# Kernel optimization log

Hardware: AMD Instinct MI355X
Metric: run time of the kernel (lower is better)

## Reference

```python
import jax, jax.numpy as jnp
import numpy as np
import math

B, S, D, H = 2, 1024, 1024, 16
DH = D // H
BUCKETS, MAXPOS = 256, 512
SPAN = BUCKETS  # pos_ebd_size (att_span)


def make_log_bucket_position(rel, bucket_size, max_position):
    sign = jnp.sign(rel).astype(jnp.float32)
    mid = bucket_size // 2
    abs_pos = jnp.where((rel < mid) & (rel > -mid), mid - 1, jnp.abs(rel)).astype(jnp.float32)
    log_pos = jnp.ceil(jnp.log(abs_pos / mid) / np.log((max_position - 1) / mid) * (mid - 1)) + mid
    return jnp.where(abs_pos <= mid, rel.astype(jnp.float32), log_pos * sign).astype(jnp.int32)


def build_relative_position(q_size, k_size):
    rel = jnp.arange(q_size, dtype=jnp.int32)[:, None] - jnp.arange(k_size, dtype=jnp.int32)[None, :]
    return make_log_bucket_position(rel, BUCKETS, MAXPOS)


def setup_inputs() -> dict:
    key = jax.random.key(0)
    ks = jax.random.split(key, 8)
    w = lambda k: jax.random.normal(k, (D, D), dtype=jnp.float32) * 0.02
    return {
        "hidden_states": jax.random.normal(ks[0], (B, S, D), dtype=jnp.float32),
        "attention_mask": jnp.ones((B, 1, S, S), dtype=jnp.int32),
        "rel_embeddings": jax.random.normal(ks[1], (2 * SPAN, D), dtype=jnp.float32),
        "Wq": w(ks[2]), "bq": jnp.zeros((D,), jnp.float32),
        "Wk": w(ks[3]), "bk": jnp.zeros((D,), jnp.float32),
        "Wv": w(ks[4]), "bv": jnp.zeros((D,), jnp.float32),
    }


def reference(hidden_states, attention_mask, rel_embeddings, Wq, bq, Wk, bk, Wv, bv):
    split = lambda x: x.reshape(B, -1, H, DH).transpose(0, 2, 1, 3)  # [B,H,S,dh]
    q = split(hidden_states @ Wq + bq)
    k = split(hidden_states @ Wk + bk)
    v = split(hidden_states @ Wv + bv)

    SCALE_FACTOR = 3  # 1 + c2p + p2c
    scale = math.sqrt(DH * SCALE_FACTOR)
    scores = jnp.einsum('bhqd,bhkd->bhqk', q, k) / scale

    # disentangled relative-position bias (share_att_key=True -> reuse q/k proj)
    re = rel_embeddings[: 2 * SPAN]  # [2*SPAN, D]
    pos_q = (re @ Wq + bq).reshape(2 * SPAN, H, DH).transpose(1, 0, 2)  # [H,P,dh]
    pos_k = (re @ Wk + bk).reshape(2 * SPAN, H, DH).transpose(1, 0, 2)

    rel_pos = build_relative_position(S, S)  # [S,S] bucketized

    # c2p: gather along the position axis per (q,k) pair
    c2p_pos = jnp.clip(rel_pos + SPAN, 0, 2 * SPAN - 1)
    c2p_att = jnp.einsum('bhqd,hpd->bhqp', q, pos_k)  # [B,H,S,2*SPAN]
    c2p = jnp.take_along_axis(c2p_att, c2p_pos[None, None], axis=-1)  # [B,H,S,S]

    # p2c: gather for key positions, then transpose back to [q,k]
    p2c_pos = jnp.clip(-rel_pos + SPAN, 0, 2 * SPAN - 1)
    p2c_att = jnp.einsum('bhkd,hpd->bhkp', k, pos_q)
    p2c = jnp.swapaxes(jnp.take_along_axis(p2c_att, p2c_pos[None, None], axis=-1), -1, -2)

    scores = scores + (c2p + p2c) / scale

    # XSoftmax: masked fill -> softmax -> zero masked
    valid = attention_mask.astype(bool)
    scores = jnp.where(valid, scores, jnp.finfo(scores.dtype).min)
    probs = jax.nn.softmax(scores, axis=-1)
    probs = jnp.where(valid, probs, 0.0)

    ctx = jnp.einsum('bhqk,bhkd->bhqd', probs, v)
    return ctx.transpose(0, 2, 1, 3).reshape(B, S, D)
```

## Files before the change

### kernel.cpp

```cpp
#include <hip/hip_runtime.h>
#include <hip/hip_bf16.h>
#include <math.h>

#define B_   2
#define S_   1024
#define D_   1024
#define H_   16
#define DH_  64
#define P_   512

#define SCALE2 (0.07216878364870323f * 1.4426950408889634f)

typedef __bf16 bf16;
typedef __bf16 bf16x8 __attribute__((ext_vector_type(8)));
typedef __bf16 bf16x4 __attribute__((ext_vector_type(4)));
typedef float  f32x4  __attribute__((ext_vector_type(4)));

__device__ __forceinline__ f32x4 mfma16(bf16x8 a, bf16x8 b, f32x4 c) {
  return __builtin_amdgcn_mfma_f32_16x16x32_bf16(a, b, c, 0, 0, 0);
}

__device__ __forceinline__ bf16x8 ld8(const bf16* p) {
  return *reinterpret_cast<const bf16x8*>(p);
}

__device__ __forceinline__ void gl_lds16(const void* g, void* l) {
  __builtin_amdgcn_global_load_lds(
      (const __attribute__((address_space(1))) void*)g,
      (__attribute__((address_space(3))) void*)l, 16, 0, 0);
}

__device__ __forceinline__ bf16x8 ld8f(const float* p) {
  const f32x4* pv = reinterpret_cast<const f32x4*>(p);
  f32x4 lo = pv[0], hi = pv[1];
  bf16x8 r;
#pragma unroll
  for (int j = 0; j < 4; j++) { r[j] = (bf16)lo[j]; r[4 + j] = (bf16)hi[j]; }
  return r;
}

__global__ __launch_bounds__(256)
void k_prep(const float* __restrict__ hidden, const float* __restrict__ re,
            const float* __restrict__ Wq, const float* __restrict__ Wk,
            const float* __restrict__ Wv,
            bf16* __restrict__ Xc, int* __restrict__ ci, bf16* __restrict__ Wt) {
  __shared__ bf16 tile[64][72];
  const int bx = blockIdx.x;
  const int t = threadIdx.x;
  if (bx < 1280) {
    int gt = bx * 256 + t;
    if (gt < 2047) {
      int rel = gt - 1023;
      int sgn = (rel > 0) - (rel < 0);
      float abs_pos = (rel < 128 && rel > -128) ? 127.0f : fabsf((float)rel);
      int bucket;
      if (abs_pos <= 128.0f) {
        bucket = rel;
      } else {
        const float logden = 1.3843393302355437f;
        float t1 = logf(abs_pos * (1.0f / 128.0f));
        float lp = ceilf(t1 / logden * 127.0f) + 128.0f;
        bucket = (int)lp * sgn;
      }
      ci[gt] = min(max(bucket + 256, 0), 511);
    }
    size_t i8 = (size_t)gt * 8;
    const size_t HN = (size_t)2048 * 1024;
    const float* src = (i8 < HN) ? (hidden + i8) : (re + (i8 - HN));
    *reinterpret_cast<bf16x8*>(&Xc[i8]) = ld8f(src);
    return;
  }
  const int bid2 = bx - 1280;
  const int w = bid2 >> 8;
  const int rem = bid2 & 255;
  const int n0 = (rem & 15) * 64;
  const int k0 = (rem >> 4) * 64;
  const float* W = (w == 0) ? Wq : (w == 1) ? Wk : Wv;
  bf16* Out = Wt + (size_t)w * D_ * D_;
  {
    const int row = t >> 2, c0 = (t & 3) * 16;
    bf16x8 v0 = ld8f(W + (size_t)(k0 + row) * D_ + n0 + c0);
    bf16x8 v1 = ld8f(W + (size_t)(k0 + row) * D_ + n0 + c0 + 8);
    *reinterpret_cast<bf16x8*>(&tile[row][c0]) = v0;
    *reinterpret_cast<bf16x8*>(&tile[row][c0 + 8]) = v1;
  }
  __syncthreads();
  {
    const int nr = t >> 2, kc0 = (t & 3) * 16;
    bf16x8 o0, o1;
#pragma unroll
    for (int j = 0; j < 8; j++) o0[j] = tile[kc0 + j][nr];
#pragma unroll
    for (int j = 0; j < 8; j++) o1[j] = tile[kc0 + 8 + j][nr];
    *reinterpret_cast<bf16x8*>(&Out[(size_t)(n0 + nr) * D_ + k0 + kc0]) = o0;
    *reinterpret_cast<bf16x8*>(&Out[(size_t)(n0 + nr) * D_ + k0 + kc0 + 8]) = o1;
  }
}

__global__ __launch_bounds__(256)
void k_proj(const bf16* __restrict__ Xc, const bf16* __restrict__ Wt,
            const float* __restrict__ bq, const float* __restrict__ bk,
            const float* __restrict__ bv,
            bf16* __restrict__ qb, bf16* __restrict__ kb, bf16* __restrict__ vbT,
            bf16* __restrict__ posq, bf16* __restrict__ posk) {
  __shared__ __align__(16) char smem[65536];
  bf16* As = reinterpret_cast<bf16*>(smem);
  bf16* Bs = reinterpret_cast<bf16*>(smem + 32768);
  const int t = threadIdx.x;
  const int w = t >> 6, lane = t & 63, quad = lane >> 4, lc = lane & 15;
  const int wm = w >> 1, wn = w & 1;
  const int m0 = blockIdx.y * 128;
  const int wsel = blockIdx.x >> 3;
  const int n0 = (blockIdx.x & 7) * 128;
  const bf16* WtW = Wt + (size_t)wsel * D_ * D_;
  const float* bias = (wsel == 0) ? bq : (wsel == 1) ? bk : bv;
  const bf16* Agl = Xc + (size_t)m0 * D_;
  const bf16* Bgl = WtW + (size_t)n0 * D_;

  int rS[8], cS[8];
#pragma unroll
  for (int i = 0; i < 8; i++) {
    int g = i * 256 + t;
    rS[i] = g >> 4;
    cS[i] = (g & 15) ^ (rS[i] & 15);
  }

  f32x4 zv = {0.f, 0.f, 0.f, 0.f};
  f32x4 acc[4][4];
#pragma unroll
  for (int i = 0; i < 4; i++)
#pragma unroll
    for (int j = 0; j < 4; j++) acc[i][j] = zv;

  for (int k0 = 0; k0 < D_; k0 += 128) {
#pragma unroll
    for (int i = 0; i < 8; i++)
      gl_lds16(Agl + (size_t)rS[i] * D_ + k0 + cS[i] * 8,
               &As[(i * 256 + w * 64) * 8]);
#pragma unroll
    for (int i = 0; i < 8; i++)
      gl_lds16(Bgl + (size_t)rS[i] * D_ + k0 + cS[i] * 8,
               &Bs[(i * 256 + w * 64) * 8]);
    __syncthreads();

#pragma unroll
    for (int h = 0; h < 4; h++) {
      bf16x8 af[4], bfr[4];
#pragma unroll
      for (int mt = 0; mt < 4; mt++) {
        int row = wm * 64 + mt * 16 + lc;
        int ch = (h * 4 + quad) ^ (row & 15);
        af[mt] = ld8(&As[row * 128 + ch * 8]);
      }
#pragma unroll
      for (int nt = 0; nt < 4; nt++) {
        int row = wn * 64 + nt * 16 + lc;
        int ch = (h * 4 + quad) ^ (row & 15);
        bfr[nt] = ld8(&Bs[row * 128 + ch * 8]);
      }
#pragma unroll
      for (int mt = 0; mt < 4; mt++)
#pragma unroll
        for (int nt = 0; nt < 4; nt++)
          acc[mt][nt] = mfma16(af[mt], bfr[nt], acc[mt][nt]);
    }
    __syncthreads();
  }

  if (wsel == 2) {
#pragma unroll
    for (int nt = 0; nt < 4; nt++) {
      int nl = n0 + wn * 64 + nt * 16 + lc;
      float bsv = bias[nl];
      int h = nl >> 6, d = nl & 63;
#pragma unroll
      for (int mt = 0; mt < 4; mt++) {
        int i0 = m0 + wm * 64 + mt * 16 + quad * 4;
        if (i0 < 2048) {
          int b = i0 >> 10, s0 = i0 & 1023;
          int spos = (s0 & ~63) | (quad * 16 + mt * 4);
          bf16x4 ov;
#pragma unroll
          for (int r = 0; r < 4; r++) ov[r] = (bf16)(acc[mt][nt][r] + bsv);
          *reinterpret_cast<bf16x4*>(
              &vbT[(((size_t)(b * H_ + h)) * DH_ + d) * S_ + spos]) = ov;
        }
      }
    }
  } else {
    bf16* Cl = reinterpret_cast<bf16*>(smem);
#pragma unroll
    for (int nt = 0; nt < 4; nt++) {
      int nl = n0 + wn * 64 + nt * 16 + lc;
      float bsv = bias[nl];
      int jl = wn * 64 + nt * 16 + lc;
#pragma unroll
      for (int mt = 0; mt < 4; mt++) {
#pragma unroll
        for (int r = 0; r < 4; r++) {
          int il = wm * 64 + mt * 16 + quad * 4 + r;
          Cl[il * 136 + jl] = (bf16)(acc[mt][nt][r] + bsv);
        }
      }
    }
    __syncthreads();
    const int hg = t >> 7;
    const int tl = t & 127;
    const int hglob = (n0 >> 6) + hg;
    bf16* dst;
    if (m0 < 2048) {
      int b = m0 >> 10, s0 = m0 & 1023;
      bf16* qk = (wsel == 0) ? qb : kb;
      dst = qk + (((size_t)(b * H_ + hglob)) * S_ + s0) * DH_;
    } else {
      int p0 = m0 - 2048;
      bf16* pm = (wsel == 0) ? posq : posk;
      dst = pm + ((size_t)hglob * P_ + p0) * DH_;
    }
#pragma unroll
    for (int rep = 0; rep < 8; rep++) {
      int u = rep * 128 + tl;
      int sl = u >> 3, dc = u & 7;
      bf16x8 v = *reinterpret_cast<const bf16x8*>(
          &Cl[sl * 136 + hg * 64 + dc * 8]);
      *reinterpret_cast<bf16x8*>(&dst[(size_t)u * 8]) = v;
    }
  }
}

__global__ __launch_bounds__(256)
void k_rel(const bf16* __restrict__ qb, const bf16* __restrict__ kb,
           const bf16* __restrict__ posq, const bf16* __restrict__ posk,
           bf16* __restrict__ c2p, bf16* __restrict__ p2c) {
  const int t = threadIdx.x;
  const int w = t >> 6, lane = t & 63, quad = lane >> 4, lc = lane & 15;
  const int which = blockIdx.z & 1;
  const int bh = blockIdx.z >> 1;
  const int h = bh & (H_ - 1);
  const int q0 = blockIdx.x * 64;
  const bf16* QK = (which ? kb : qb) + (size_t)bh * S_ * DH_;
  const bf16* PM = (which ? posq : posk) + (size_t)h * P_ * DH_;
  bf16* Out = (which ? p2c : c2p) + (size_t)bh * S_ * P_;

  f32x4 zv = {0.f, 0.f, 0.f, 0.f};
  bf16x8 bq[4][2];
#pragma unroll
  for (int qi = 0; qi < 4; qi++) {
    const bf16* qp = QK + (size_t)(q0 + qi * 16 + lc) * DH_ + quad * 8;
    bq[qi][0] = ld8(qp);
    bq[qi][1] = ld8(qp + 32);
  }
  const int p0 = w * 128;
#pragma unroll 2
  for (int pt = 0; pt < 8; pt++) {
    const bf16* pp = PM + (size_t)(p0 + pt * 16 + lc) * DH_ + quad * 8;
    bf16x8 pa0 = ld8(pp), pa1 = ld8(pp + 32);
#pragma unroll
    for (int qi = 0; qi < 4; qi++) {
      f32x4 acc = mfma16(pa1, bq[qi][1], mfma16(pa0, bq[qi][0], zv));
      int q = q0 + qi * 16 + lc;
      int pbase = p0 + pt * 16 + quad * 4;
      bf16x4 ov;
#pragma unroll
      for (int r = 0; r < 4; r++) ov[r] = (bf16)acc[r];
      *reinterpret_cast<bf16x4*>(&Out[(size_t)q * P_ + pbase]) = ov;
    }
  }
}

__global__ __launch_bounds__(256, 2)
void k_attn(const bf16* __restrict__ qb, const bf16* __restrict__ kb,
            const bf16* __restrict__ vbT, const bf16* __restrict__ c2p,
            const bf16* __restrict__ p2c, const int* __restrict__ citab,
            float* __restrict__ out) {
  __shared__ bf16 c2pS[64 * 136];
  __shared__ bf16 p2cS[64 * 136];
  __shared__ bf16 vT0[64 * 64];
  __shared__ bf16 vT1[64 * 64];
  __shared__ int  ciT[2048];

  const int t = threadIdx.x;
  const int w = t >> 6, lane = t & 63, quad = lane >> 4, lc = lane & 15;
  const int bh = blockIdx.x;
  const int q0 = blockIdx.y * 64;

  const bf16* qp = qb + ((size_t)bh * S_ + q0 + w * 16 + lc) * DH_ + quad * 8;
  bf16x8 aq0 = ld8(qp), aq1 = ld8(qp + 32);

  const bf16* kbB = kb + (size_t)bh * S_ * DH_;
  const bf16* vbB = vbT + (size_t)bh * DH_ * S_;
  const bf16* c2pB = c2p + (size_t)bh * S_ * P_;
  const bf16* p2cB = p2c + (size_t)bh * S_ * P_;

#pragma unroll
  for (int i = 0; i < 2; i++)
    gl_lds16((const char*)citab + (size_t)(i * 256 + t) * 16,
             (char*)ciT + (i * 256 + w * 64) * 16);

  int wrow[5], wch[5];
#pragma unroll
  for (int i = 0; i < 5; i++) {
    int slot = i * 256 + ((i == 4) ? (t & 63) : t);
    wrow[i] = slot / 17;
    wch[i] = slot - wrow[i] * 17;
  }
  int vrow[2], vch[2];
#pragma unroll
  for (int i = 0; i < 2; i++) {
    int slot = i * 256 + t;
    vrow[i] = slot >> 3;
    vch[i] = (slot & 7) ^ (vrow[i] & 7);
  }

  f32x4 zv = {0.f, 0.f, 0.f, 0.f};
  float m_r = -INFINITY, l_r = 0.f;
  f32x4 oacc[4];
#pragma unroll
  for (int dg = 0; dg < 4; dg++) oacc[dg] = zv;

  const int jbase2 = w * 16 + lc + 63 - quad * 4;
  const int qoff = (w * 16 + lc) * 136;
  int poff[4];
#pragma unroll
  for (int g = 0; g < 4; g++) poff[g] = (g * 16 + quad * 4) * 136;

  __syncthreads();

  int clo8_cur = ciT[q0 + 960] & ~7;
#pragma unroll
  for (int i = 0; i < 4; i++) {
    gl_lds16(c2pB + (size_t)(q0 + wrow[i]) * P_ + clo8_cur + wch[i] * 8,
             &c2pS[(i * 256 + w * 64) * 8]);
    gl_lds16(p2cB + (size_t)(0 + wrow[i]) * P_ + clo8_cur + wch[i] * 8,
             &p2cS[(i * 256 + w * 64) * 8]);
  }
  if (w == 0) {
    gl_lds16(c2pB + (size_t)(q0 + wrow[4]) * P_ + clo8_cur + wch[4] * 8,
             &c2pS[1024 * 8]);
    gl_lds16(p2cB + (size_t)(0 + wrow[4]) * P_ + clo8_cur + wch[4] * 8,
             &p2cS[1024 * 8]);
  }
#pragma unroll
  for (int i = 0; i < 2; i++)
    gl_lds16(vbB + (size_t)vrow[i] * S_ + 0 + vch[i] * 8,
             &vT0[(i * 256 + w * 64) * 8]);

  bf16x8 kf[4][2];
#pragma unroll
  for (int g = 0; g < 4; g++) {
    const bf16* kp = kbB + (size_t)(g * 16 + lc) * DH_ + quad * 8;
    kf[g][0] = ld8(kp);
    kf[g][1] = ld8(kp + 32);
  }

  int buf = 0;
  for (int kt = 0; kt < S_; kt += 64) {
    __syncthreads();

    int idxn = q0 - kt + 896;
    const int clo8n = ciT[idxn < 0 ? 0 : idxn] & ~7;

    const int ktn = (kt + 64 < S_) ? kt + 64 : 0;
    bf16x8 kfn[4][2];
#pragma unroll
    for (int g = 0; g < 4; g++) {
      const bf16* kp = kbB + (size_t)(ktn + g * 16 + lc) * DH_ + quad * 8;
      kfn[g][0] = ld8(kp);
      kfn[g][1] = ld8(kp + 32);
    }

    f32x4 s[4];
#pragma unroll
    for (int g = 0; g < 4; g++)
      s[g] = mfma16(kf[g][1], aq1, mfma16(kf[g][0], aq0, zv));

    const int jb = q0 - kt + 960 + jbase2;
    int jj[4][4];
#pragma unroll
    for (int g = 0; g < 4; g++)
#pragma unroll
      for (int r = 0; r < 4; r++)
        jj[g][r] = ciT[jb - 16 * g - r] - clo8_cur;
    float cvv[4][4], pvv[4][4];
#pragma unroll
    for (int g = 0; g < 4; g++)
#pragma unroll
      for (int r = 0; r < 4; r++) {
        cvv[g][r] = (float)c2pS[qoff + jj[g][r]];
        pvv[g][r] = (float)p2cS[poff[g] + r * 136 + jj[g][r]];
      }
#pragma unroll
    for (int g = 0; g < 4; g++)
#pragma unroll
      for (int r = 0; r < 4; r++)
        s[g][r] = (s[g][r] + cvv[g][r] + pvv[g][r]) * SCALE2;

    __syncthreads();

    if (kt + 64 < S_) {
      bf16* vnext = buf ? vT0 : vT1;
#pragma unroll
      for (int i = 0; i < 4; i++) {
        gl_lds16(c2pB + (size_t)(q0 + wrow[i]) * P_ + clo8n + wch[i] * 8,
                 &c2pS[(i * 256 + w * 64) * 8]);
        gl_lds16(p2cB + (size_t)(kt + 64 + wrow[i]) * P_ + clo8n + wch[i] * 8,
                 &p2cS[(i * 256 + w * 64) * 8]);
      }
      if (w == 0) {
        gl_lds16(c2pB + (size_t)(q0 + wrow[4]) * P_ + clo8n + wch[4] * 8,
                 &c2pS[1024 * 8]);
        gl_lds16(p2cB + (size_t)(kt + 64 + wrow[4]) * P_ + clo8n + wch[4] * 8,
                 &p2cS[1024 * 8]);
      }
#pragma unroll
      for (int i = 0; i < 2; i++)
        gl_lds16(vbB + (size_t)vrow[i] * S_ + kt + 64 + vch[i] * 8,
                 &vnext[(i * 256 + w * 64) * 8]);
    }

    const bf16* vcur = buf ? vT1 : vT0;
    bf16x8 va0a[4], va1a[4];
#pragma unroll
    for (int dg = 0; dg < 4; dg++) {
      int row = dg * 16 + lc;
      va0a[dg] = ld8(&vcur[row * 64 + ((2 * quad) ^ (row & 7)) * 8]);
      va1a[dg] = ld8(&vcur[row * 64 + ((2 * quad + 1) ^ (row & 7)) * 8]);
    }

    float mx;
    {
      float m0 = fmaxf(fmaxf(s[0][0], s[0][1]), fmaxf(s[0][2], s[0][3]));
      float m1 = fmaxf(fmaxf(s[1][0], s[1][1]), fmaxf(s[1][2], s[1][3]));
      float m2 = fmaxf(fmaxf(s[2][0], s[2][1]), fmaxf(s[2][2], s[2][3]));
      float m3 = fmaxf(fmaxf(s[3][0], s[3][1]), fmaxf(s[3][2], s[3][3]));
      mx = fmaxf(fmaxf(m0, m1), fmaxf(m2, m3));
    }
    mx = fmaxf(mx, __shfl_xor(mx, 16));
    mx = fmaxf(mx, __shfl_xor(mx, 32));
    float mnew = fmaxf(m_r, mx);
    float alpha = exp2f(m_r - mnew);
    m_r = mnew;
    float ps = 0.f;
#pragma unroll
    for (int g = 0; g < 4; g++)
#pragma unroll
      for (int r = 0; r < 4; r++) {
        float pe = exp2f(s[g][r] - mnew);
        s[g][r] = pe;
        ps += pe;
      }
    ps += __shfl_xor(ps, 16);
    ps += __shfl_xor(ps, 32);
    l_r = l_r * alpha + ps;
#pragma unroll
    for (int dg = 0; dg < 4; dg++)
#pragma unroll
      for (int r = 0; r < 4; r++) oacc[dg][r] *= alpha;

    bf16x8 pb0, pb1;
#pragma unroll
    for (int e = 0; e < 8; e++) {
      pb0[e] = (bf16)s[e >> 2][e & 3];
      pb1[e] = (bf16)s[2 + (e >> 2)][e & 3];
    }

#pragma unroll
    for (int dg = 0; dg < 4; dg++)
      oacc[dg] = mfma16(va1a[dg], pb1, mfma16(va0a[dg], pb0, oacc[dg]));

    clo8_cur = clo8n;
#pragma unroll
    for (int g = 0; g < 4; g++) { kf[g][0] = kfn[g][0]; kf[g][1] = kfn[g][1]; }
    buf ^= 1;
  }

  const int b = bh >> 4, h = bh & 15;
  const float inv = 1.0f / l_r;
  const int qa = q0 + w * 16 + lc;
#pragma unroll
  for (int dg = 0; dg < 4; dg++) {
    f32x4 ov;
#pragma unroll
    for (int r = 0; r < 4; r++) ov[r] = oacc[dg][r] * inv;
    *reinterpret_cast<f32x4*>(
        &out[((size_t)(b * S_) + qa) * D_ + h * DH_ + dg * 16 + quad * 4]) = ov;
  }
}

extern "C" void kernel_launch(void* const* d_in, const int* in_sizes, int n_in,
                              void* d_out, int out_size, void* d_ws,
                              size_t ws_size, hipStream_t stream) {
  const float* hidden = (const float*)d_in[0];
  const float* re = (const float*)d_in[2];
  const float* Wq = (const float*)d_in[3];
  const float* bq = (const float*)d_in[4];
  const float* Wk = (const float*)d_in[5];
  const float* bk = (const float*)d_in[6];
  const float* Wv = (const float*)d_in[7];
  const float* bv = (const float*)d_in[8];

  char* ws = (char*)d_ws;
  const size_t MB = 1024 * 1024;
  bf16* qb   = (bf16*)(ws + 0 * MB);
  bf16* kb   = (bf16*)(ws + 4 * MB);
  bf16* vbT  = (bf16*)(ws + 8 * MB);
  bf16* posq = (bf16*)(ws + 12 * MB);
  bf16* posk = (bf16*)(ws + 13 * MB);
  int*  ci   = (int*) (ws + 14 * MB);
  bf16* Wt   = (bf16*)(ws + 15 * MB);
  bf16* c2p  = (bf16*)(ws + 26 * MB);
  bf16* p2c  = (bf16*)(ws + 58 * MB);
  bf16* Xc   = (bf16*)(ws + 26 * MB);
  if (ws_size < 92 * MB) return;

  k_prep<<<dim3(2048), dim3(256), 0, stream>>>(hidden, re, Wq, Wk, Wv,
                                               Xc, ci, Wt);
  k_proj<<<dim3(24, 20), dim3(256), 0, stream>>>(Xc, Wt, bq, bk, bv,
                                                 qb, kb, vbT, posq, posk);
  k_rel<<<dim3(16, 1, 64), dim3(256), 0, stream>>>(qb, kb, posq, posk, c2p, p2c);
  k_attn<<<dim3(32, 16), dim3(256), 0, stream>>>(qb, kb, vbT, c2p, p2c, ci,
                                                 (float*)d_out);
}
```

Measured before the change: 194.4 us.

## Use lazy softmax rescaling, MFMA row sums, and prefetched gather indices

The online softmax now rescales the running max and accumulators only when some lane's tile max exceeds the stored max by more than 8 (log2 units). This removes the per-tile cross-lane max shuffles and the alpha rescale in the common case. The row sum is accumulated with an extra MFMA against a vector of ones, using the bf16-rounded probabilities, which replaces the scalar sum and its shuffles. The relative-position gather indices for the next tile are computed one iteration ahead so the LDS index loads are off the critical path. In exchange there is a wave-wide branch, more registers for the prefetched indices, and exponentials that can reach 2^8 before a rescale.

Result: no change. 197.4 us (+1.5%).

```diff
diff --git a/kernel.cpp b/kernel.cpp
--- a/kernel.cpp
+++ b/kernel.cpp
@@ -313,10 +313,14 @@
   }
 
   f32x4 zv = {0.f, 0.f, 0.f, 0.f};
-  float m_r = -INFINITY, l_r = 0.f;
+  float m_r = -INFINITY;
   f32x4 oacc[4];
+  f32x4 lacc = zv;
 #pragma unroll
   for (int dg = 0; dg < 4; dg++) oacc[dg] = zv;
+  bf16x8 ones8;
+#pragma unroll
+  for (int j = 0; j < 8; j++) ones8[j] = (bf16)1.0f;
 
   const int jbase2 = w * 16 + lc + 63 - quad * 4;
   const int qoff = (w * 16 + lc) * 136;
@@ -327,6 +331,14 @@
   __syncthreads();
 
   int clo8_cur = ciT[q0 + 960] & ~7;
+  int jj[4][4];
+  {
+    const int jb0 = q0 + 960 + jbase2;
+#pragma unroll
+    for (int g = 0; g < 4; g++)
+#pragma unroll
+      for (int r = 0; r < 4; r++) jj[g][r] = ciT[jb0 - 16 * g - r] - clo8_cur;
+  }
 #pragma unroll
   for (int i = 0; i < 4; i++) {
     gl_lds16(c2pB + (size_t)(q0 + wrow[i]) * P_ + clo8_cur + wch[i] * 8,
@@ -374,13 +386,6 @@
     for (int g = 0; g < 4; g++)
       s[g] = mfma16(kf[g][1], aq1, mfma16(kf[g][0], aq0, zv));
 
-    const int jb = q0 - kt + 960 + jbase2;
-    int jj[4][4];
-#pragma unroll
-    for (int g = 0; g < 4; g++)
-#pragma unroll
-      for (int r = 0; r < 4; r++)
-        jj[g][r] = ciT[jb - 16 * g - r] - clo8_cur;
     float cvv[4][4], pvv[4][4];
 #pragma unroll
     for (int g = 0; g < 4; g++)
@@ -394,6 +399,18 @@
 #pragma unroll
       for (int r = 0; r < 4; r++)
         s[g][r] = (s[g][r] + cvv[g][r] + pvv[g][r]) * SCALE2;
+
+    int jjn[4][4];
+    {
+      const int jbn = q0 - kt + 896 + jbase2;
+#pragma unroll
+      for (int g = 0; g < 4; g++)
+#pragma unroll
+        for (int r = 0; r < 4; r++) {
+          int ix = jbn - 16 * g - r;
+          jjn[g][r] = ciT[ix < 0 ? 0 : ix] - clo8n;
+        }
+    }
 
     __syncthreads();
 
@@ -427,35 +444,31 @@
       va1a[dg] = ld8(&vcur[row * 64 + ((2 * quad + 1) ^ (row & 7)) * 8]);
     }
 
-    float mx;
+    float lm;
     {
       float m0 = fmaxf(fmaxf(s[0][0], s[0][1]), fmaxf(s[0][2], s[0][3]));
       float m1 = fmaxf(fmaxf(s[1][0], s[1][1]), fmaxf(s[1][2], s[1][3]));
       float m2 = fmaxf(fmaxf(s[2][0], s[2][1]), fmaxf(s[2][2], s[2][3]));
       float m3 = fmaxf(fmaxf(s[3][0], s[3][1]), fmaxf(s[3][2], s[3][3]));
-      mx = fmaxf(fmaxf(m0, m1), fmaxf(m2, m3));
-    }
-    mx = fmaxf(mx, __shfl_xor(mx, 16));
-    mx = fmaxf(mx, __shfl_xor(mx, 32));
-    float mnew = fmaxf(m_r, mx);
-    float alpha = exp2f(m_r - mnew);
-    m_r = mnew;
-    float ps = 0.f;
+      lm = fmaxf(fmaxf(m0, m1), fmaxf(m2, m3));
+    }
+    if (__any(lm > m_r + 8.0f)) {
+      float rm = fmaxf(lm, __shfl_xor(lm, 16));
+      rm = fmaxf(rm, __shfl_xor(rm, 32));
+      float mnew = fmaxf(m_r, rm);
+      float alpha = exp2f(m_r - mnew);
+      m_r = mnew;
+#pragma unroll
+      for (int dg = 0; dg < 4; dg++)
+#pragma unroll
+        for (int r = 0; r < 4; r++) oacc[dg][r] *= alpha;
+#pragma unroll
+      for (int r = 0; r < 4; r++) lacc[r] *= alpha;
+    }
 #pragma unroll
     for (int g = 0; g < 4; g++)
 #pragma unroll
-      for (int r = 0; r < 4; r++) {
-        float pe = exp2f(s[g][r] - mnew);
-        s[g][r] = pe;
-        ps += pe;
-      }
-    ps += __shfl_xor(ps, 16);
-    ps += __shfl_xor(ps, 32);
-    l_r = l_r * alpha + ps;
-#pragma unroll
-    for (int dg = 0; dg < 4; dg++)
-#pragma unroll
-      for (int r = 0; r < 4; r++) oacc[dg][r] *= alpha;
+      for (int r = 0; r < 4; r++) s[g][r] = exp2f(s[g][r] - m_r);
 
     bf16x8 pb0, pb1;
 #pragma unroll
@@ -467,15 +480,20 @@
 #pragma unroll
     for (int dg = 0; dg < 4; dg++)
       oacc[dg] = mfma16(va1a[dg], pb1, mfma16(va0a[dg], pb0, oacc[dg]));
+    lacc = mfma16(ones8, pb1, mfma16(ones8, pb0, lacc));
 
     clo8_cur = clo8n;
 #pragma unroll
     for (int g = 0; g < 4; g++) { kf[g][0] = kfn[g][0]; kf[g][1] = kfn[g][1]; }
+#pragma unroll
+    for (int g = 0; g < 4; g++)
+#pragma unroll
+      for (int r = 0; r < 4; r++) jj[g][r] = jjn[g][r];
     buf ^= 1;
   }
 
   const int b = bh >> 4, h = bh & 15;
-  const float inv = 1.0f / l_r;
+  const float inv = 1.0f / lacc[0];
   const int qa = q0 + w * 16 + lc;
 #pragma unroll
   for (int dg = 0; dg < 4; dg++) {
```
